# Kernel tuning notes

Hardware: AMD Instinct MI355X
Metric: run time of the kernel (lower is better)

The kernel has to match this reference:

```python
import jax, jax.numpy as jnp
import numpy as np

TIMESTEPS = 32
INITIAL_THRESHOLD = 0.5
ADAPTATION_RATE = 0.1


def setup_inputs() -> dict:
    key = jax.random.key(0)
    x = jax.random.uniform(key, (32, 65536), dtype=jnp.float32)
    return {"x": x}


def reference(x):
    # Adaptive threshold spike encoding.
    # State: accumulated input and per-element threshold; scanned over timesteps.
    thr0 = jnp.full(x.shape, INITIAL_THRESHOLD, dtype=x.dtype)
    acc0 = jnp.zeros_like(x)
    rate = ADAPTATION_RATE
    adapt = rate * jnp.abs(x)  # constant across timesteps

    def step(carry, _):
        acc, thr = carry
        acc = acc + x
        mask = acc >= thr
        spikes_t = mask.astype(x.dtype)
        acc = jnp.where(mask, jnp.zeros_like(acc), acc)
        thr = thr * (1.0 - rate) + adapt
        return (acc, thr), spikes_t

    _, spikes = jax.lax.scan(step, (acc0, thr0), None, length=TIMESTEPS)
    # spikes: [T, B, F] -> [B, T, F]
    return jnp.moveaxis(spikes, 0, 1)
```

## Files before the change

kernel.cpp:

```cpp
#include <hip/hip_runtime.h>


#define TSTEPS 32
#define BDIM 32
#define FDIM 65536

typedef float floatx4 __attribute__((ext_vector_type(4)));

__global__ __launch_bounds__(256) void spike_fma_f32_nt_kernel(
    const float* __restrict__ x, float* __restrict__ out) {
    int gid = blockIdx.x * blockDim.x + threadIdx.x;
    int fi  = gid & (FDIM / 4 - 1);
    int b   = gid >> 14;
    int f   = fi << 2;

    const floatx4 xv = *reinterpret_cast<const floatx4*>(x + (size_t)b * FDIM + f);
    float xs[4] = {xv.x, xv.y, xv.z, xv.w};

    float acc[4], thr[4], ad[4];
#pragma unroll
    for (int i = 0; i < 4; ++i) {
        acc[i] = 0.0f;
        thr[i] = 0.5f;
        ad[i]  = 0.1f * fabsf(xs[i]);
    }

    float* outb = out + (size_t)b * TSTEPS * FDIM + f;

#pragma unroll
    for (int t = 0; t < TSTEPS; ++t) {
        floatx4 sp;
#pragma unroll
        for (int e = 0; e < 4; ++e) {
            acc[e] = acc[e] + xs[e];
            bool m = acc[e] >= thr[e];
            sp[e]  = m ? 1.0f : 0.0f;
            acc[e] = m ? 0.0f : acc[e];
            thr[e] = __builtin_fmaf(thr[e], 0.9f, ad[e]);
        }
        __builtin_nontemporal_store(
            sp, reinterpret_cast<floatx4*>(outb + (size_t)t * FDIM));
    }
}

extern "C" void kernel_launch(void* const* d_in, const int* in_sizes, int n_in,
                              void* d_out, int out_size, void* d_ws, size_t ws_size,
                              hipStream_t stream) {
    (void)in_sizes; (void)n_in; (void)d_ws; (void)ws_size; (void)out_size;
    const float* x = (const float*)d_in[0];
    float* out     = (float*)d_out;
    const int total_threads = BDIM * FDIM / 4;
    spike_fma_f32_nt_kernel<<<total_threads / 256, 256, 0, stream>>>(x, out);
}
```

Baseline: 265.7 us.

## Split spike encoding into bit-packed compute pass and float expansion pass

```diff
diff --git a/kernel.cpp b/kernel.cpp
--- a/kernel.cpp
+++ b/kernel.cpp
@@ -7,7 +7,65 @@
 
 typedef float floatx4 __attribute__((ext_vector_type(4)));
 
-__global__ __launch_bounds__(256) void spike_fma_f32_nt_kernel(
+__global__ __launch_bounds__(256) void spike_bits_kernel(
+    const float* __restrict__ x, unsigned char* __restrict__ bits) {
+    int tid = blockIdx.x * blockDim.x + threadIdx.x;
+    int fb  = tid & 8191;
+    int b   = tid >> 13;
+
+    const float* xb = x + ((size_t)b << 16) + ((size_t)fb << 3);
+    const floatx4 v0 = *reinterpret_cast<const floatx4*>(xb);
+    const floatx4 v1 = *reinterpret_cast<const floatx4*>(xb + 4);
+
+    float xs[8], acc[8], thr[8], ad[8];
+#pragma unroll
+    for (int e = 0; e < 8; ++e) {
+        xs[e]  = (e < 4) ? v0[e] : v1[e - 4];
+        acc[e] = 0.0f;
+        thr[e] = 0.5f;
+        ad[e]  = 0.1f * fabsf(xs[e]);
+    }
+
+    unsigned char* ob = bits + (((size_t)b * TSTEPS) << 13) + fb;
+
+#pragma unroll
+    for (int t = 0; t < TSTEPS; ++t) {
+        unsigned m8 = 0;
+#pragma unroll
+        for (int e = 0; e < 8; ++e) {
+            acc[e] = acc[e] + xs[e];
+            bool m = acc[e] >= thr[e];
+            m8 |= (m ? 1u : 0u) << e;
+            acc[e] = m ? 0.0f : acc[e];
+            thr[e] = __builtin_fmaf(thr[e], 0.9f, ad[e]);
+        }
+        ob[(size_t)t << 13] = (unsigned char)m8;
+    }
+}
+
+__global__ __launch_bounds__(256) void spike_expand_kernel(
+    const unsigned char* __restrict__ bits, float* __restrict__ out) {
+    int gid = blockIdx.x * blockDim.x + threadIdx.x;
+    int t   = gid >> 14;
+    int f   = (gid << 2) & (FDIM - 1);
+
+    const unsigned char* bp = bits + ((size_t)t << 13) + (f >> 3);
+    const int sh = f & 7;
+    float* op = out + ((size_t)gid << 2);
+
+#pragma unroll 8
+    for (int b = 0; b < BDIM; ++b) {
+        unsigned nib = ((unsigned)bp[(size_t)b << 18] >> sh) & 0xFu;
+        floatx4 sp;
+        sp.x = (nib & 1u) ? 1.0f : 0.0f;
+        sp.y = (nib & 2u) ? 1.0f : 0.0f;
+        sp.z = (nib & 4u) ? 1.0f : 0.0f;
+        sp.w = (nib & 8u) ? 1.0f : 0.0f;
+        *reinterpret_cast<floatx4*>(op + ((size_t)b << 21)) = sp;
+    }
+}
+
+__global__ __launch_bounds__(256) void spike_fma_f32_kernel(
     const float* __restrict__ x, float* __restrict__ out) {
     int gid = blockIdx.x * blockDim.x + threadIdx.x;
     int fi  = gid & (FDIM / 4 - 1);
@@ -20,13 +78,9 @@
     float acc[4], thr[4], ad[4];
 #pragma unroll
     for (int i = 0; i < 4; ++i) {
-        acc[i] = 0.0f;
-        thr[i] = 0.5f;
-        ad[i]  = 0.1f * fabsf(xs[i]);
+        acc[i] = 0.0f; thr[i] = 0.5f; ad[i] = 0.1f * fabsf(xs[i]);
     }
-
     float* outb = out + (size_t)b * TSTEPS * FDIM + f;
-
 #pragma unroll
     for (int t = 0; t < TSTEPS; ++t) {
         floatx4 sp;
@@ -38,17 +92,22 @@
             acc[e] = m ? 0.0f : acc[e];
             thr[e] = __builtin_fmaf(thr[e], 0.9f, ad[e]);
         }
-        __builtin_nontemporal_store(
-            sp, reinterpret_cast<floatx4*>(outb + (size_t)t * FDIM));
+        *reinterpret_cast<floatx4*>(outb + (size_t)t * FDIM) = sp;
     }
 }
 
 extern "C" void kernel_launch(void* const* d_in, const int* in_sizes, int n_in,
                               void* d_out, int out_size, void* d_ws, size_t ws_size,
                               hipStream_t stream) {
-    (void)in_sizes; (void)n_in; (void)d_ws; (void)ws_size; (void)out_size;
+    (void)in_sizes; (void)n_in; (void)out_size;
     const float* x = (const float*)d_in[0];
     float* out     = (float*)d_out;
-    const int total_threads = BDIM * FDIM / 4;
-    spike_fma_f32_nt_kernel<<<total_threads / 256, 256, 0, stream>>>(x, out);
+    const size_t bits_bytes = (size_t)BDIM * TSTEPS * (FDIM / 8);
+    if (d_ws != nullptr && ws_size >= bits_bytes) {
+        unsigned char* bits = (unsigned char*)d_ws;
+        spike_bits_kernel<<<BDIM * FDIM / 8 / 256, 256, 0, stream>>>(x, bits);
+        spike_expand_kernel<<<BDIM * FDIM / 4 / 256, 256, 0, stream>>>(bits, out);
+    } else {
+        spike_fma_f32_kernel<<<BDIM * FDIM / 4 / 256, 256, 0, stream>>>(x, out);
+    }
 }
```

Result: slower. 285.5 us (+7.4%).
